# Optimization experiments

Hardware: AMD Instinct MI355X
Metric: run time of the kernel (lower is better)

Reference implementation:

```python
import jax, jax.numpy as jnp
import numpy as np

D_MODEL = 1024
HEADS = 16
D_K = D_MODEL // HEADS  # 64


def setup_inputs() -> dict:
    key = jax.random.key(0)
    ks = jax.random.split(key, 9)
    B, S = 4, 2048
    values = jax.random.normal(ks[0], (B, S, D_MODEL), dtype=jnp.float32)
    keys = jax.random.normal(ks[1], (B, S, D_MODEL), dtype=jnp.float32)
    query = jax.random.normal(ks[2], (B, S, D_MODEL), dtype=jnp.float32)
    mask = jax.random.randint(ks[3], (1, 1, S, S), 0, 2, dtype=jnp.int32)
    # per-head projection weights (shared across heads), torch Linear layout (out, in)
    sc = 1.0 / np.sqrt(D_K)
    Wv = jax.random.uniform(ks[4], (D_K, D_K), jnp.float32, -sc, sc)
    Wk = jax.random.uniform(ks[5], (D_K, D_K), jnp.float32, -sc, sc)
    Wq = jax.random.uniform(ks[6], (D_K, D_K), jnp.float32, -sc, sc)
    so = 1.0 / np.sqrt(D_MODEL)
    Wo = jax.random.uniform(ks[7], (D_MODEL, D_MODEL), jnp.float32, -so, so)
    bo = jax.random.uniform(ks[8], (D_MODEL,), jnp.float32, -so, so)
    return {"values": values, "keys": keys, "query": query, "mask": mask,
            "Wv": Wv, "Wk": Wk, "Wq": Wq, "Wo": Wo, "bo": bo}


def reference(values, keys, query, mask, Wv, Wk, Wq, Wo, bo):
    n, q_len, d = query.shape
    v_len, k_len = values.shape[1], keys.shape[1]
    # reshape to (n, len, heads, d_k) and apply shared per-head linear (x @ W^T)
    v = values.reshape(n, v_len, HEADS, D_K) @ Wv.T
    k = keys.reshape(n, k_len, HEADS, D_K) @ Wk.T
    q = query.reshape(n, q_len, HEADS, D_K) @ Wq.T
    # scores: (n, h, q, k)
    scores = jnp.einsum('nqhd,nkhd->nhqk', q, k)
    scores = jnp.where(mask == 0, jnp.float32(-1e20), scores)
    attn = jax.nn.softmax(scores / jnp.sqrt(jnp.float32(D_K)), axis=3)
    out = jnp.einsum('nhqk,nkhd->nqhd', attn, v).reshape(n, q_len, HEADS * D_K)
    return out @ Wo.T + bo
```

## Files before the change

kernel.cpp:

```cpp
#include <hip/hip_runtime.h>

#define B 4
#define S 2048
#define H 16
#define DK 64
#define DM 1024
#define NTILES (S / 64)
#define QSCALE 0.18033688011112042f

typedef _Float16 half_t;
typedef __attribute__((ext_vector_type(8))) _Float16 half8v;
typedef __attribute__((ext_vector_type(2))) __fp16   fp16x2;
typedef __attribute__((ext_vector_type(4))) float    float4v;

__device__ __forceinline__ unsigned pkh(float lo, float hi) {
    union { fp16x2 h; unsigned u; } cvt;
    cvt.h = __builtin_amdgcn_cvt_pkrtz(lo, hi);
    return cvt.u;
}
__device__ __forceinline__ float fast_exp2(float x) {
#if __has_builtin(__builtin_amdgcn_exp2f)
    return __builtin_amdgcn_exp2f(x);
#else
    return __expf(x * 0.69314718055994531f);
#endif
}
__device__ __forceinline__ half8v cvt8h(float4 a, float4 b) {
    half8v r;
    r[0] = (half_t)a.x; r[1] = (half_t)a.y; r[2] = (half_t)a.z; r[3] = (half_t)a.w;
    r[4] = (half_t)b.x; r[5] = (half_t)b.y; r[6] = (half_t)b.z; r[7] = (half_t)b.w;
    return r;
}
__device__ __forceinline__ void gl2lds16(const void* g, void* l) {
    __builtin_amdgcn_global_load_lds(
        (const __attribute__((address_space(1))) unsigned int*)g,
        (__attribute__((address_space(3))) unsigned int*)l, 16, 0, 0);
}

#define MASK_BLOCKS (S * S / 256)
__global__ __launch_bounds__(256) void prep_kernel(
    const int* __restrict__ mask, unsigned long long* __restrict__ mp,
    const float* __restrict__ Wo, half_t* __restrict__ Wh)
{
    int bx = blockIdx.x;
    if (bx < MASK_BLOCKS) {
        int t = bx * 256 + threadIdx.x;
        int m = mask[t];
        unsigned long long b = __ballot(m != 0);
        if ((threadIdx.x & 63) == 0) mp[t >> 6] = b;
    } else {
        int t = ((bx - MASK_BLOCKS) * 256 + threadIdx.x) * 4;
        float4 wv = *(const float4*)(Wo + t);
        union { half_t h[4]; uint2 u; } cvt;
        cvt.h[0] = (half_t)wv.x; cvt.h[1] = (half_t)wv.y;
        cvt.h[2] = (half_t)wv.z; cvt.h[3] = (half_t)wv.w;
        *(uint2*)(Wh + t) = cvt.u;
    }
}

__global__ __launch_bounds__(256) void qkv_proj_kernel(
    const float* __restrict__ xv, const float* __restrict__ xk, const float* __restrict__ xq,
    const float* __restrict__ Wv, const float* __restrict__ Wk, const float* __restrict__ Wq,
    half_t* __restrict__ vtw, half_t* __restrict__ kw, half_t* __restrict__ qw)
{
    const int y = blockIdx.y;
    const float* x; const float* W;
    if (y == 0)      { x = xv; W = Wv; }
    else if (y == 1) { x = xk; W = Wk; }
    else             { x = xq; W = Wq; }

    const int tid = threadIdx.x;
    const int w = tid >> 6, L = tid & 63, a = L & 15, g = L >> 4;
    const int bx  = blockIdx.x;
    const int st  = bx & 31;
    const int bh  = bx >> 5;
    const int b_  = bh >> 4, h = bh & 15;
    const int s0b = st * 64;

    half8v wF[4][2];
    #pragma unroll
    for (int t = 0; t < 4; ++t)
        #pragma unroll
        for (int c = 0; c < 2; ++c) {
            const float* wr = W + (size_t)(16 * t + a) * 64 + 32 * c + 8 * g;
            wF[t][c] = cvt8h(*(const float4*)wr, *(const float4*)(wr + 4));
        }

    const float* xr = x + ((size_t)(b_ * S) + s0b + 16 * w + a) * DM + h * 64 + 8 * g;
    half8v xF0 = cvt8h(*(const float4*)(xr),      *(const float4*)(xr + 4));
    half8v xF1 = cvt8h(*(const float4*)(xr + 32), *(const float4*)(xr + 36));

    const float4v z4 = {0.0f, 0.0f, 0.0f, 0.0f};

    if (y == 0) {
        const int c   = 16 * w + a;
        const int pos = 32 * (c >> 5) + 8 * ((c >> 2) & 3) + 4 * ((c >> 4) & 1) + (c & 3);
        #pragma unroll
        for (int mt = 0; mt < 4; ++mt) {
            float4v D = __builtin_amdgcn_mfma_f32_16x16x32_f16(wF[mt][0], xF0, z4, 0, 0, 0);
            D = __builtin_amdgcn_mfma_f32_16x16x32_f16(wF[mt][1], xF1, D, 0, 0, 0);
            #pragma unroll
            for (int r = 0; r < 4; ++r)
                vtw[((size_t)bh * 64 + 16 * mt + 4 * g + r) * S + s0b + pos] = (half_t)D[r];
        }
    } else {
        half_t* out = (y == 1) ? kw : qw;
        const float scale = (y == 2) ? QSCALE : 1.0f;
        #pragma unroll
        for (int nt = 0; nt < 4; ++nt) {
            float4v D = __builtin_amdgcn_mfma_f32_16x16x32_f16(xF0, wF[nt][0], z4, 0, 0, 0);
            D = __builtin_amdgcn_mfma_f32_16x16x32_f16(xF1, wF[nt][1], D, 0, 0, 0);
            #pragma unroll
            for (int r = 0; r < 4; ++r)
                out[((size_t)bh * S + s0b + 16 * w + 4 * g + r) * 64 + 16 * nt + a] =
                    (half_t)(D[r] * scale);
        }
    }
}

__global__ __launch_bounds__(256) void flash_attn_kernel(
    const half_t* __restrict__ q, const half_t* __restrict__ k,
    const half_t* __restrict__ vt, const unsigned long long* __restrict__ mp,
    half_t* __restrict__ att)
{
    __shared__ half_t KV[2][2][64 * 64];

    const int tid = threadIdx.x;
    const int w   = tid >> 6;
    const int L   = tid & 63;
    const int a   = L & 15;
    const int g   = L >> 4;
    const int bh  = blockIdx.x;
    const int b_  = bh >> 4, h = bh & 15;
    const int qs  = blockIdx.y * 256 + w * 64;

    const half_t* qb = q  + (size_t)bh * S * 64;
    const half_t* kb = k  + (size_t)bh * S * 64;
    const half_t* vb = vt + (size_t)bh * 64 * S;

    half8v qB[4][2];
    #pragma unroll
    for (int gq = 0; gq < 4; ++gq) {
        const half_t* qr = qb + (size_t)(qs + 16 * gq + a) * 64;
        qB[gq][0] = *(const half8v*)(qr +      g * 8);
        qB[gq][1] = *(const half8v*)(qr + 32 + g * 8);
    }

    const unsigned long long* mr[4];
    #pragma unroll
    for (int gq = 0; gq < 4; ++gq)
        mr[gq] = mp + (size_t)(qs + 16 * gq + a) * NTILES;

    int srow[2], schk[2];
    #pragma unroll
    for (int i = 0; i < 2; ++i) {
        int p   = (w * 2 + i) * 64 + L;
        srow[i] = p >> 3;
        schk[i] = (p & 7) ^ (srow[i] & 7);
    }

    half8v ones;
    #pragma unroll
    for (int i = 0; i < 8; ++i) ones[i] = (half_t)1.0f;

    const float4v z4 = {0.0f, 0.0f, 0.0f, 0.0f};
    float4v o[4][4];
    #pragma unroll
    for (int gq = 0; gq < 4; ++gq)
        #pragma unroll
        for (int nt = 0; nt < 4; ++nt) o[gq][nt] = z4;
    float4v lD[4] = {z4, z4, z4, z4};

    #pragma unroll
    for (int i = 0; i < 2; ++i) {
        gl2lds16(kb + (size_t)srow[i] * 64 + schk[i] * 8, &KV[0][0][(w * 2 + i) * 64 * 8]);
        gl2lds16(vb + (size_t)srow[i] * S + schk[i] * 8,  &KV[0][1][(w * 2 + i) * 64 * 8]);
    }

    for (int kt = 0; kt < NTILES; ++kt) {
        const int cur = kt & 1;
        __syncthreads();

        if (kt + 1 < NTILES) {
            const int nk = kt + 1;
            #pragma unroll
            for (int i = 0; i < 2; ++i) {
                gl2lds16(kb + ((size_t)(nk * 64 + srow[i])) * 64 + schk[i] * 8,
                         &KV[cur ^ 1][0][(w * 2 + i) * 64 * 8]);
                gl2lds16(vb + (size_t)srow[i] * S + nk * 64 + schk[i] * 8,
                         &KV[cur ^ 1][1][(w * 2 + i) * 64 * 8]);
            }
        }

        unsigned long long mw[4];
        #pragma unroll
        for (int gq = 0; gq < 4; ++gq) mw[gq] = mr[gq][kt];

        const half_t* Kb = &KV[cur][0][0];
        const half_t* Vb = &KV[cur][1][0];

        half8v kB[4][2], vA[4][2];
        #pragma unroll
        for (int nt = 0; nt < 4; ++nt)
            #pragma unroll
            for (int c = 0; c < 2; ++c) {
                const int off = ((16 * nt + a) * 8 + ((4 * c + g) ^ (a & 7))) * 8;
                kB[nt][c] = *(const half8v*)(Kb + off);
                vA[nt][c] = *(const half8v*)(Vb + off);
            }

        #pragma unroll
        for (int gq = 0; gq < 4; ++gq) {
            float4v st[4];
            #pragma unroll
            for (int nt = 0; nt < 4; ++nt) {
                st[nt] = __builtin_amdgcn_mfma_f32_16x16x32_f16(kB[nt][0], qB[gq][0], z4, 0, 0, 0);
                st[nt] = __builtin_amdgcn_mfma_f32_16x16x32_f16(kB[nt][1], qB[gq][1], st[nt], 0, 0, 0);
            }

            float e[4][4];
            #pragma unroll
            for (int nt = 0; nt < 4; ++nt) {
                unsigned bnt = (unsigned)(mw[gq] >> (16 * nt + 4 * g));
                #pragma unroll
                for (int r = 0; r < 4; ++r) {
                    float ee = fast_exp2(st[nt][r]);
                    e[nt][r] = ((bnt >> r) & 1u) ? ee : 0.0f;
                }
            }

            half8v pB[2];
            #pragma unroll
            for (int c = 0; c < 2; ++c) {
                union { unsigned u[4]; half8v hv; } cvt;
                cvt.u[0] = pkh(e[2*c  ][0], e[2*c  ][1]);
                cvt.u[1] = pkh(e[2*c  ][2], e[2*c  ][3]);
                cvt.u[2] = pkh(e[2*c+1][0], e[2*c+1][1]);
                cvt.u[3] = pkh(e[2*c+1][2], e[2*c+1][3]);
                pB[c] = cvt.hv;
            }

            #pragma unroll
            for (int nt = 0; nt < 4; ++nt) {
                o[gq][nt] = __builtin_amdgcn_mfma_f32_16x16x32_f16(vA[nt][0], pB[0], o[gq][nt], 0, 0, 0);
                o[gq][nt] = __builtin_amdgcn_mfma_f32_16x16x32_f16(vA[nt][1], pB[1], o[gq][nt], 0, 0, 0);
            }
            lD[gq] = __builtin_amdgcn_mfma_f32_16x16x32_f16(ones, pB[0], lD[gq], 0, 0, 0);
            lD[gq] = __builtin_amdgcn_mfma_f32_16x16x32_f16(ones, pB[1], lD[gq], 0, 0, 0);
        }
    }

    #pragma unroll
    for (int gq = 0; gq < 4; ++gq) {
        const float inv = 1.0f / lD[gq][0];
        const size_t row = (size_t)(b_ * S + qs + 16 * gq + a);
        #pragma unroll
        for (int nt = 0; nt < 4; ++nt) {
            union { unsigned u[2]; uint2 u2; } cvt;
            cvt.u[0] = pkh(o[gq][nt][0] * inv, o[gq][nt][1] * inv);
            cvt.u[1] = pkh(o[gq][nt][2] * inv, o[gq][nt][3] * inv);
            *(uint2*)(att + row * DM + h * 64 + 16 * nt + 4 * g) = cvt.u2;
        }
    }
}

__global__ __launch_bounds__(256, 2) void out_proj_kernel(
    const half_t* __restrict__ X, const half_t* __restrict__ Wh,
    const float* __restrict__ bo, float* __restrict__ out)
{
    __shared__ half_t SA[2][128 * 64], SB[2][128 * 64];

    const int tid = threadIdx.x;
    const int w = tid >> 6, L = tid & 63, a = L & 15, g = L >> 4;
    const int wm = w >> 1, wn = w & 1;
    const int r0 = blockIdx.x * 128;
    const int n0 = blockIdx.y * 128;

    int prow[4], pchk[4], pbase[4];
    #pragma unroll
    for (int i = 0; i < 4; ++i) {
        int p    = w * 256 + i * 64 + L;
        prow[i]  = p >> 3;
        pchk[i]  = (p & 7) ^ (prow[i] & 7);
        pbase[i] = (w * 256 + i * 64) * 8;
    }

    const float4v z4 = {0.0f, 0.0f, 0.0f, 0.0f};
    float4v acc[4][4];
    #pragma unroll
    for (int mt = 0; mt < 4; ++mt)
        #pragma unroll
        for (int nt = 0; nt < 4; ++nt) acc[mt][nt] = z4;

    #pragma unroll
    for (int i = 0; i < 4; ++i) {
        gl2lds16(X  + (size_t)(r0 + prow[i]) * DM + pchk[i] * 8, &SA[0][pbase[i]]);
        gl2lds16(Wh + (size_t)(n0 + prow[i]) * DM + pchk[i] * 8, &SB[0][pbase[i]]);
    }

    for (int kt = 0; kt < DM / 64; ++kt) {
        const int cur = kt & 1;
        __syncthreads();

        if (kt + 1 < DM / 64) {
            const int k0 = (kt + 1) * 64;
            #pragma unroll
            for (int i = 0; i < 4; ++i) {
                gl2lds16(X  + (size_t)(r0 + prow[i]) * DM + k0 + pchk[i] * 8, &SA[cur ^ 1][pbase[i]]);
                gl2lds16(Wh + (size_t)(n0 + prow[i]) * DM + k0 + pchk[i] * 8, &SB[cur ^ 1][pbase[i]]);
            }
        }

        half8v bF[4][2];
        #pragma unroll
        for (int nt = 0; nt < 4; ++nt)
            #pragma unroll
            for (int c = 0; c < 2; ++c) {
                const int rb  = 64 * wn + 16 * nt + a;
                const int off = (rb * 8 + ((4 * c + g) ^ (rb & 7))) * 8;
                bF[nt][c] = *(const half8v*)&SB[cur][off];
            }

        #pragma unroll
        for (int mt = 0; mt < 4; ++mt) {
            const int ra   = 64 * wm + 16 * mt + a;
            const int off0 = (ra * 8 + ((0 + g) ^ (ra & 7))) * 8;
            const int off1 = (ra * 8 + ((4 + g) ^ (ra & 7))) * 8;
            half8v a0 = *(const half8v*)&SA[cur][off0];
            half8v a1 = *(const half8v*)&SA[cur][off1];
            #pragma unroll
            for (int nt = 0; nt < 4; ++nt) {
                float4v acv = acc[mt][nt];
                acv = __builtin_amdgcn_mfma_f32_16x16x32_f16(a0, bF[nt][0], acv, 0, 0, 0);
                acv = __builtin_amdgcn_mfma_f32_16x16x32_f16(a1, bF[nt][1], acv, 0, 0, 0);
                acc[mt][nt] = acv;
            }
        }
    }

    #pragma unroll
    for (int mt = 0; mt < 4; ++mt) {
        const int m0 = r0 + 64 * wm + 16 * mt + 4 * g;
        #pragma unroll
        for (int nt = 0; nt < 4; ++nt) {
            const int n = n0 + 64 * wn + 16 * nt + a;
            const float bias = bo[n];
            #pragma unroll
            for (int r = 0; r < 4; ++r)
                out[(size_t)(m0 + r) * DM + n] = acc[mt][nt][r] + bias;
        }
    }
}

extern "C" void kernel_launch(void* const* d_in, const int* in_sizes, int n_in,
                              void* d_out, int out_size, void* d_ws, size_t ws_size,
                              hipStream_t stream) {
    (void)in_sizes; (void)n_in; (void)out_size; (void)ws_size;
    const float* values = (const float*)d_in[0];
    const float* keys   = (const float*)d_in[1];
    const float* query  = (const float*)d_in[2];
    const int*   mask   = (const int*)d_in[3];
    const float* Wv     = (const float*)d_in[4];
    const float* Wk     = (const float*)d_in[5];
    const float* Wq     = (const float*)d_in[6];
    const float* Wo     = (const float*)d_in[7];
    const float* bo     = (const float*)d_in[8];
    float* out = (float*)d_out;

    const size_t per = (size_t)B * H * S * DK;
    half_t* qw  = (half_t*)d_ws;
    half_t* kw  = qw + per;
    half_t* vtw = kw + per;
    unsigned long long* mp = (unsigned long long*)(vtw + per);
    half_t* atth = (half_t*)(mp + (size_t)S * S / 64);
    half_t* woh  = atth + per;

    prep_kernel<<<MASK_BLOCKS + DM * DM / 1024, 256, 0, stream>>>(mask, mp, Wo, woh);

    dim3 g1(B * H * (S / 64), 3);
    qkv_proj_kernel<<<g1, 256, 0, stream>>>(values, keys, query, Wv, Wk, Wq, vtw, kw, qw);

    dim3 g2(B * H, S / 256);
    flash_attn_kernel<<<g2, 256, 0, stream>>>(qw, kw, vtw, mp, atth);

    dim3 g3(B * S / 128, DM / 128);
    out_proj_kernel<<<g3, 256, 0, stream>>>(atth, woh, bo, out);
}
```

Baseline: 328.1 us.

## Stage QKV projection output through LDS and split flash attention across eight waves

The QKV projection kernel now writes MFMA results into a padded shared-memory tile and then stores them to global memory with 16-byte vectorized, row-contiguous writes, replacing scattered 2-byte stores. The flash attention kernel moves to 512 threads per block, and each wave now handles 32 query rows instead of 64. Each thread issues one K/V async load per tile instead of two. This halves per-wave register state (accumulators, Q fragments) to allow more waves in flight, at the cost of each wave reloading K/V fragments from LDS for fewer queries.

```diff
diff --git a/kernel.cpp b/kernel.cpp
--- a/kernel.cpp
+++ b/kernel.cpp
@@ -58,11 +58,14 @@
     }
 }
 
+#define QSTR 72
 __global__ __launch_bounds__(256) void qkv_proj_kernel(
     const float* __restrict__ xv, const float* __restrict__ xk, const float* __restrict__ xq,
     const float* __restrict__ Wv, const float* __restrict__ Wk, const float* __restrict__ Wq,
     half_t* __restrict__ vtw, half_t* __restrict__ kw, half_t* __restrict__ qw)
 {
+    __shared__ half_t Ls[64 * QSTR];
+
     const int y = blockIdx.y;
     const float* x; const float* W;
     if (y == 0)      { x = xv; W = Wv; }
@@ -101,10 +104,9 @@
             D = __builtin_amdgcn_mfma_f32_16x16x32_f16(wF[mt][1], xF1, D, 0, 0, 0);
             #pragma unroll
             for (int r = 0; r < 4; ++r)
-                vtw[((size_t)bh * 64 + 16 * mt + 4 * g + r) * S + s0b + pos] = (half_t)D[r];
+                Ls[(16 * mt + 4 * g + r) * QSTR + pos] = (half_t)D[r];
         }
     } else {
-        half_t* out = (y == 1) ? kw : qw;
         const float scale = (y == 2) ? QSCALE : 1.0f;
         #pragma unroll
         for (int nt = 0; nt < 4; ++nt) {
@@ -112,13 +114,26 @@
             D = __builtin_amdgcn_mfma_f32_16x16x32_f16(xF1, wF[nt][1], D, 0, 0, 0);
             #pragma unroll
             for (int r = 0; r < 4; ++r)
-                out[((size_t)bh * S + s0b + 16 * w + 4 * g + r) * 64 + 16 * nt + a] =
-                    (half_t)(D[r] * scale);
-        }
-    }
-}
-
-__global__ __launch_bounds__(256) void flash_attn_kernel(
+                Ls[(16 * w + 4 * g + r) * QSTR + 16 * nt + a] = (half_t)(D[r] * scale);
+        }
+    }
+    __syncthreads();
+
+    const int row = tid >> 2;
+    const int col = (tid & 3) * 16;
+    uint4 v0 = *(const uint4*)&Ls[row * QSTR + col];
+    uint4 v1 = *(const uint4*)&Ls[row * QSTR + col + 8];
+    half_t* dst;
+    if (y == 0)      dst = vtw + ((size_t)bh * 64 + row) * S + s0b + col;
+    else {
+        half_t* out = (y == 1) ? kw : qw;
+        dst = out + ((size_t)bh * S + s0b + row) * 64 + col;
+    }
+    *(uint4*)dst = v0;
+    *(uint4*)(dst + 8) = v1;
+}
+
+__global__ __launch_bounds__(512) void flash_attn_kernel(
     const half_t* __restrict__ q, const half_t* __restrict__ k,
     const half_t* __restrict__ vt, const unsigned long long* __restrict__ mp,
     half_t* __restrict__ att)
@@ -132,50 +147,39 @@
     const int g   = L >> 4;
     const int bh  = blockIdx.x;
     const int b_  = bh >> 4, h = bh & 15;
-    const int qs  = blockIdx.y * 256 + w * 64;
+    const int qs  = blockIdx.y * 256 + w * 32;
 
     const half_t* qb = q  + (size_t)bh * S * 64;
     const half_t* kb = k  + (size_t)bh * S * 64;
     const half_t* vb = vt + (size_t)bh * 64 * S;
 
-    half8v qB[4][2];
-    #pragma unroll
-    for (int gq = 0; gq < 4; ++gq) {
+    half8v qB[2][2];
+    #pragma unroll
+    for (int gq = 0; gq < 2; ++gq) {
         const half_t* qr = qb + (size_t)(qs + 16 * gq + a) * 64;
         qB[gq][0] = *(const half8v*)(qr +      g * 8);
         qB[gq][1] = *(const half8v*)(qr + 32 + g * 8);
     }
 
-    const unsigned long long* mr[4];
-    #pragma unroll
-    for (int gq = 0; gq < 4; ++gq)
+    const unsigned long long* mr[2];
+    #pragma unroll
+    for (int gq = 0; gq < 2; ++gq)
         mr[gq] = mp + (size_t)(qs + 16 * gq + a) * NTILES;
 
-    int srow[2], schk[2];
-    #pragma unroll
-    for (int i = 0; i < 2; ++i) {
-        int p   = (w * 2 + i) * 64 + L;
-        srow[i] = p >> 3;
-        schk[i] = (p & 7) ^ (srow[i] & 7);
-    }
+    const int p    = w * 64 + L;
+    const int srow = p >> 3;
+    const int schk = (p & 7) ^ (srow & 7);
 
     half8v ones;
     #pragma unroll
     for (int i = 0; i < 8; ++i) ones[i] = (half_t)1.0f;
 
     const float4v z4 = {0.0f, 0.0f, 0.0f, 0.0f};
-    float4v o[4][4];
-    #pragma unroll
-    for (int gq = 0; gq < 4; ++gq)
-        #pragma unroll
-        for (int nt = 0; nt < 4; ++nt) o[gq][nt] = z4;
-    float4v lD[4] = {z4, z4, z4, z4};
-
-    #pragma unroll
-    for (int i = 0; i < 2; ++i) {
-        gl2lds16(kb + (size_t)srow[i] * 64 + schk[i] * 8, &KV[0][0][(w * 2 + i) * 64 * 8]);
-        gl2lds16(vb + (size_t)srow[i] * S + schk[i] * 8,  &KV[0][1][(w * 2 + i) * 64 * 8]);
-    }
+    float4v o[2][4] = {{z4, z4, z4, z4}, {z4, z4, z4, z4}};
+    float4v lD[2] = {z4, z4};
+
+    gl2lds16(kb + (size_t)srow * 64 + schk * 8, &KV[0][0][w * 512]);
+    gl2lds16(vb + (size_t)srow * S + schk * 8,  &KV[0][1][w * 512]);
 
     for (int kt = 0; kt < NTILES; ++kt) {
         const int cur = kt & 1;
@@ -183,18 +187,15 @@
 
         if (kt + 1 < NTILES) {
             const int nk = kt + 1;
-            #pragma unroll
-            for (int i = 0; i < 2; ++i) {
-                gl2lds16(kb + ((size_t)(nk * 64 + srow[i])) * 64 + schk[i] * 8,
-                         &KV[cur ^ 1][0][(w * 2 + i) * 64 * 8]);
-                gl2lds16(vb + (size_t)srow[i] * S + nk * 64 + schk[i] * 8,
-                         &KV[cur ^ 1][1][(w * 2 + i) * 64 * 8]);
-            }
-        }
-
-        unsigned long long mw[4];
-        #pragma unroll
-        for (int gq = 0; gq < 4; ++gq) mw[gq] = mr[gq][kt];
+            gl2lds16(kb + ((size_t)(nk * 64 + srow)) * 64 + schk * 8,
+                     &KV[cur ^ 1][0][w * 512]);
+            gl2lds16(vb + (size_t)srow * S + nk * 64 + schk * 8,
+                     &KV[cur ^ 1][1][w * 512]);
+        }
+
+        unsigned long long mw[2];
+        #pragma unroll
+        for (int gq = 0; gq < 2; ++gq) mw[gq] = mr[gq][kt];
 
         const half_t* Kb = &KV[cur][0][0];
         const half_t* Vb = &KV[cur][1][0];
@@ -210,7 +211,7 @@
             }
 
         #pragma unroll
-        for (int gq = 0; gq < 4; ++gq) {
+        for (int gq = 0; gq < 2; ++gq) {
             float4v st[4];
             #pragma unroll
             for (int nt = 0; nt < 4; ++nt) {
@@ -251,7 +252,7 @@
     }
 
     #pragma unroll
-    for (int gq = 0; gq < 4; ++gq) {
+    for (int gq = 0; gq < 2; ++gq) {
         const float inv = 1.0f / lD[gq][0];
         const size_t row = (size_t)(b_ * S + qs + 16 * gq + a);
         #pragma unroll
@@ -381,7 +382,7 @@
     qkv_proj_kernel<<<g1, 256, 0, stream>>>(values, keys, query, Wv, Wk, Wq, vtw, kw, qw);
 
     dim3 g2(B * H, S / 256);
-    flash_attn_kernel<<<g2, 256, 0, stream>>>(qw, kw, vtw, mp, atth);
+    flash_attn_kernel<<<g2, 512, 0, stream>>>(qw, kw, vtw, mp, atth);
 
     dim3 g3(B * S / 128, DM / 128);
     out_proj_kernel<<<g3, 256, 0, stream>>>(atth, woh, bo, out);
```

Result: faster. 312.2 us (-4.8%).
